# Kernel tuning notes

Measured on AMD Instinct MI355X. Metric: run time of the kernel, lower is better.

## Reference

```python
import jax, jax.numpy as jnp
import numpy as np

N = 50000        # nodes
E = 800000       # edges
G = 256          # graphs in batch
DIMS = [128, 128, 64, 32]
BN_EPS = 1e-5
TEMP = 5.0


def setup_inputs() -> dict:
    key = jax.random.key(0)
    ks = iter(jax.random.split(key, 32))
    inp = {}
    inp["x"] = jax.random.normal(next(ks), (N, DIMS[0]), dtype=jnp.float32)
    inp["edge_index"] = jax.random.randint(next(ks), (2, E), 0, N)
    inp["batch"] = jnp.sort(jax.random.randint(next(ks), (N,), 0, G))
    for i in range(3):
        din, dout = DIMS[i], DIMS[i + 1]
        inp[f"W1_{i}"] = jax.random.normal(next(ks), (din, dout), dtype=jnp.float32) * 0.05
        inp[f"b1_{i}"] = jnp.zeros((dout,), jnp.float32)
        inp[f"W2_{i}"] = jax.random.normal(next(ks), (dout, dout), dtype=jnp.float32) * 0.05
        inp[f"b2_{i}"] = jnp.zeros((dout,), jnp.float32)
        inp[f"gamma_{i}"] = jnp.ones((dout,), jnp.float32)
        inp[f"beta_{i}"] = jnp.zeros((dout,), jnp.float32)
        inp[f"mean_{i}"] = jnp.zeros((dout,), jnp.float32)
        inp[f"var_{i}"] = jnp.ones((dout,), jnp.float32)
    inp["W_lin"] = jax.random.normal(next(ks), (DIMS[3], 1), dtype=jnp.float32) * 0.05
    inp["b_lin"] = jnp.zeros((1,), jnp.float32)
    return inp


def _gin_bn(x, src, dst, W1, b1, W2, b2, g, b, m, v):
    # GINConv with eps=0: h_i = MLP(x_i + sum_{j->i} x_j), then BatchNorm (eval)
    agg = jax.ops.segment_sum(x[src], dst, num_segments=N)  # [N, din]
    h = x + agg
    h = jnp.maximum(h @ W1 + b1, 0.0) @ W2 + b2             # 2-layer MLP
    return (h - m) * jax.lax.rsqrt(v + BN_EPS) * g + b


def reference(x, edge_index, batch,
              W1_0, b1_0, W2_0, b2_0, gamma_0, beta_0, mean_0, var_0,
              W1_1, b1_1, W2_1, b2_1, gamma_1, beta_1, mean_1, var_1,
              W1_2, b1_2, W2_2, b2_2, gamma_2, beta_2, mean_2, var_2,
              W_lin, b_lin):
    src, dst = edge_index[0], edge_index[1]
    layers = [
        (W1_0, b1_0, W2_0, b2_0, gamma_0, beta_0, mean_0, var_0),
        (W1_1, b1_1, W2_1, b2_1, gamma_1, beta_1, mean_1, var_1),
        (W1_2, b1_2, W2_2, b2_2, gamma_2, beta_2, mean_2, var_2),
    ]
    for i, p in enumerate(layers):
        x = _gin_bn(x, src, dst, *p)
        if i != len(layers) - 1:
            x = jnp.maximum(x, 0.0)  # relu; dropout is identity in eval mode
    logits = (x @ W_lin + b_lin) / TEMP                      # [N, 1]
    # per-graph (segment) softmax over nodes
    mx = jax.ops.segment_max(logits, batch, num_segments=G)  # [G, 1]
    e = jnp.exp(logits - mx[batch])
    s = jax.ops.segment_sum(e, batch, num_segments=G)        # [G, 1]
    return e / s[batch]
```

## Files before the change

### kernel.cpp

```cpp
#include <hip/hip_runtime.h>

#define NN 50000
#define NE 800000
#define NG 256
#define NB ((NN + 255) / 256)
#define N4 (NN * 128 / 4)

typedef __attribute__((ext_vector_type(8))) short bf16x8;
typedef __attribute__((ext_vector_type(4))) float f32x4;

__device__ __forceinline__ unsigned short f2bf_rne(float f) {
    unsigned u = __float_as_uint(f);
    u += 0x7fffu + ((u >> 16) & 1u);
    return (unsigned short)(u >> 16);
}
#define BF2F_LO(u) __uint_as_float((u) << 16)
#define BF2F_HI(u) __uint_as_float((u) & 0xffff0000u)

__global__ void conv_hist(const float4* __restrict__ x, ushort4* __restrict__ xh,
                          const int* __restrict__ dst, int* __restrict__ deg,
                          int* __restrict__ eoff) {
    int i = blockIdx.x * 256 + threadIdx.x;
    if (i < N4) {
        float4 v = x[i];
        ushort4 o;
        o.x = f2bf_rne(v.x); o.y = f2bf_rne(v.y);
        o.z = f2bf_rne(v.z); o.w = f2bf_rne(v.w);
        xh[i] = o;
    }
    if (i < NE) eoff[i] = atomicAdd(&deg[dst[i]], 1);
}

__global__ void block_scan(const int* __restrict__ deg, int* __restrict__ iscan,
                           int* __restrict__ bsum,
                           const float* __restrict__ W1, const float* __restrict__ W2,
                           const float* __restrict__ W3,
                           const float* __restrict__ W21, const float* __restrict__ W12,
                           unsigned short* __restrict__ W1t,
                           unsigned short* __restrict__ W2t,
                           unsigned short* __restrict__ W3t,
                           unsigned short* __restrict__ W21t,
                           unsigned short* __restrict__ W12t) {
    int gidx = blockIdx.x * 256 + threadIdx.x;
    if (gidx < 16384) {
        int n = gidx >> 7, k = gidx & 127;
        W1t[gidx] = f2bf_rne(W1[k * 128 + n]);
        W2t[gidx] = f2bf_rne(W2[k * 128 + n]);
    } else if (gidx < 24576) {
        int i2 = gidx - 16384;
        int n = i2 >> 7, k = i2 & 127;
        W3t[i2] = f2bf_rne(W3[k * 64 + n]);
    } else if (gidx < 28672) {
        int i3 = gidx - 24576;
        int n = i3 >> 6, k = i3 & 63;
        W21t[i3] = f2bf_rne(W21[k * 64 + n]);
    } else if (gidx < 30720) {
        int i4 = gidx - 28672;
        int n = i4 >> 6, k = i4 & 63;
        W12t[i4] = f2bf_rne(W12[k * 32 + n]);
    }

    __shared__ int sh[256];
    int t = threadIdx.x;
    int i = blockIdx.x * 256 + t;
    int v = (i < NN) ? deg[i] : 0;
    sh[t] = v;
    __syncthreads();
    #pragma unroll
    for (int off = 1; off < 256; off <<= 1) {
        int add = (t >= off) ? sh[t - off] : 0;
        __syncthreads();
        sh[t] += add;
        __syncthreads();
    }
    if (i < NN) iscan[i] = sh[t];
    if (t == 255) bsum[blockIdx.x] = sh[255];
}

__global__ void scan_bsum(const int* __restrict__ bsum, int* __restrict__ boff) {
    __shared__ int sh[256];
    int t = threadIdx.x;
    int v = (t < NB) ? bsum[t] : 0;
    sh[t] = v;
    __syncthreads();
    #pragma unroll
    for (int off = 1; off < 256; off <<= 1) {
        int add = (t >= off) ? sh[t - off] : 0;
        __syncthreads();
        sh[t] += add;
        __syncthreads();
    }
    if (t < NB) boff[t] = sh[t] - v;
}

__global__ void finalize_bounds(const int* __restrict__ deg, const int* __restrict__ iscan,
                                const int* __restrict__ boff, int* __restrict__ rowptr,
                                const int* __restrict__ batch, int* __restrict__ gstart) {
    int i = blockIdx.x * 256 + threadIdx.x;
    if (i < NN) {
        rowptr[i] = iscan[i] - deg[i] + boff[blockIdx.x];
        int b = batch[i];
        if (i == 0) {
            for (int g = 0; g <= b; g++) gstart[g] = 0;
        } else {
            int p = batch[i - 1];
            for (int g = p + 1; g <= b; g++) gstart[g] = i;
        }
        if (i == NN - 1) {
            for (int g = b + 1; g <= NG; g++) gstart[g] = NN;
        }
    }
    if (i == 0) rowptr[NN] = NE;
}

__global__ void fill_csr2(const int* __restrict__ src, const int* __restrict__ dst,
                          const int* __restrict__ rowptr, const int* __restrict__ eoff,
                          int* __restrict__ esrc) {
    int e = blockIdx.x * blockDim.x + threadIdx.x;
    if (e >= NE) return;
    esrc[rowptr[dst[e]] + eoff[e]] = src[e];
}


template <int C4>
__device__ __forceinline__ void gather_bf16(const uint4* __restrict__ x4,
                                            const int* __restrict__ esrc,
                                            int beg, int cnt, int node, int lane,
                                            float* a ) {
    constexpr int EPI = 64 / C4;
    const int chunk = lane & (C4 - 1);
    const int esl   = lane / C4;
    #define ACC_U4(u) do { \
        a[0] += BF2F_LO((u).x); a[1] += BF2F_HI((u).x); \
        a[2] += BF2F_LO((u).y); a[3] += BF2F_HI((u).y); \
        a[4] += BF2F_LO((u).z); a[5] += BF2F_HI((u).z); \
        a[6] += BF2F_LO((u).w); a[7] += BF2F_HI((u).w); } while (0)
    if (esl == 0) { uint4 u = x4[(size_t)node * C4 + chunk]; ACC_U4(u); }
    for (int c = 0; c < cnt; c += 64) {
        int take = min(64, cnt - c);
        int myi = (lane < take) ? esrc[beg + c + lane] : 0;
        int i = 0;
        for (; i + 4 * EPI <= take; i += 4 * EPI) {
            int s0 = __shfl(myi, i + esl);
            int s1 = __shfl(myi, i + EPI + esl);
            int s2 = __shfl(myi, i + 2 * EPI + esl);
            int s3 = __shfl(myi, i + 3 * EPI + esl);
            uint4 u0 = x4[(size_t)s0 * C4 + chunk];
            uint4 u1 = x4[(size_t)s1 * C4 + chunk];
            uint4 u2 = x4[(size_t)s2 * C4 + chunk];
            uint4 u3 = x4[(size_t)s3 * C4 + chunk];
            ACC_U4(u0); ACC_U4(u1); ACC_U4(u2); ACC_U4(u3);
        }
        if (i + 2 * EPI <= take) {
            int s0 = __shfl(myi, i + esl);
            int s1 = __shfl(myi, i + EPI + esl);
            uint4 u0 = x4[(size_t)s0 * C4 + chunk];
            uint4 u1 = x4[(size_t)s1 * C4 + chunk];
            ACC_U4(u0); ACC_U4(u1);
            i += 2 * EPI;
        }
        if (i + EPI <= take) {
            int s = __shfl(myi, i + esl);
            uint4 u = x4[(size_t)s * C4 + chunk];
            ACC_U4(u);
            i += EPI;
        }
        int rem = take - i;
        if (rem > 0) {
            int s = __shfl(myi, i + ((esl < rem) ? esl : 0));
            uint4 u = x4[(size_t)s * C4 + chunk];
            if (esl < rem) ACC_U4(u);
        }
    }
    #undef ACC_U4
    for (int off = 32; off >= C4; off >>= 1) {
        #pragma unroll
        for (int q = 0; q < 8; q++)
            a[q] += __shfl_xor(a[q], off);
    }
}

template <int C>
__device__ __forceinline__ void gather_bf16_u2(const uint2* __restrict__ x2,
                                               const int* __restrict__ esrc,
                                               int beg, int cnt, int node, int lane,
                                               float* a ) {
    constexpr int EPI = 64 / C;
    const int chunk = lane & (C - 1);
    const int esl   = lane / C;
    #define ACC_U2(u) do { \
        a[0] += BF2F_LO((u).x); a[1] += BF2F_HI((u).x); \
        a[2] += BF2F_LO((u).y); a[3] += BF2F_HI((u).y); } while (0)
    if (esl == 0) { uint2 u = x2[(size_t)node * C + chunk]; ACC_U2(u); }
    for (int c = 0; c < cnt; c += 64) {
        int take = min(64, cnt - c);
        int myi = (lane < take) ? esrc[beg + c + lane] : 0;
        int i = 0;
        for (; i + 4 * EPI <= take; i += 4 * EPI) {
            int s0 = __shfl(myi, i + esl);
            int s1 = __shfl(myi, i + EPI + esl);
            int s2 = __shfl(myi, i + 2 * EPI + esl);
            int s3 = __shfl(myi, i + 3 * EPI + esl);
            uint2 u0 = x2[(size_t)s0 * C + chunk];
            uint2 u1 = x2[(size_t)s1 * C + chunk];
            uint2 u2 = x2[(size_t)s2 * C + chunk];
            uint2 u3 = x2[(size_t)s3 * C + chunk];
            ACC_U2(u0); ACC_U2(u1); ACC_U2(u2); ACC_U2(u3);
        }
        if (i + 2 * EPI <= take) {
            int s0 = __shfl(myi, i + esl);
            int s1 = __shfl(myi, i + EPI + esl);
            uint2 u0 = x2[(size_t)s0 * C + chunk];
            uint2 u1 = x2[(size_t)s1 * C + chunk];
            ACC_U2(u0); ACC_U2(u1);
            i += 2 * EPI;
        }
        if (i + EPI <= take) {
            int s = __shfl(myi, i + esl);
            uint2 u = x2[(size_t)s * C + chunk];
            ACC_U2(u);
            i += EPI;
        }
        int rem = take - i;
        if (rem > 0) {
            int s = __shfl(myi, i + ((esl < rem) ? esl : 0));
            uint2 u = x2[(size_t)s * C + chunk];
            if (esl < rem) ACC_U2(u);
        }
    }
    #undef ACC_U2
    for (int off = 32; off >= C; off >>= 1) {
        #pragma unroll
        for (int q = 0; q < 4; q++)
            a[q] += __shfl_xor(a[q], off);
    }
}

template <int C>
__device__ __forceinline__ void gather_bf16_u1(const unsigned* __restrict__ x1,
                                               const int* __restrict__ esrc,
                                               int beg, int cnt, int node, int lane,
                                               float* a ) {
    constexpr int EPI = 64 / C;
    const int chunk = lane & (C - 1);
    const int esl   = lane / C;
    #define ACC_U1(u) do { \
        a[0] += BF2F_LO(u); a[1] += BF2F_HI(u); } while (0)
    if (esl == 0) { unsigned u = x1[(size_t)node * C + chunk]; ACC_U1(u); }
    for (int c = 0; c < cnt; c += 64) {
        int take = min(64, cnt - c);
        int myi = (lane < take) ? esrc[beg + c + lane] : 0;
        int i = 0;
        for (; i + 4 * EPI <= take; i += 4 * EPI) {
            int s0 = __shfl(myi, i + esl);
            int s1 = __shfl(myi, i + EPI + esl);
            int s2 = __shfl(myi, i + 2 * EPI + esl);
            int s3 = __shfl(myi, i + 3 * EPI + esl);
            unsigned u0 = x1[(size_t)s0 * C + chunk];
            unsigned u1 = x1[(size_t)s1 * C + chunk];
            unsigned u2 = x1[(size_t)s2 * C + chunk];
            unsigned u3 = x1[(size_t)s3 * C + chunk];
            ACC_U1(u0); ACC_U1(u1); ACC_U1(u2); ACC_U1(u3);
        }
        if (i + 2 * EPI <= take) {
            int s0 = __shfl(myi, i + esl);
            int s1 = __shfl(myi, i + EPI + esl);
            unsigned u0 = x1[(size_t)s0 * C + chunk];
            unsigned u1 = x1[(size_t)s1 * C + chunk];
            ACC_U1(u0); ACC_U1(u1);
            i += 2 * EPI;
        }
        if (i + EPI <= take) {
            int s = __shfl(myi, i + esl);
            unsigned u = x1[(size_t)s * C + chunk];
            ACC_U1(u);
            i += EPI;
        }
        int rem = take - i;
        if (rem > 0) {
            int s = __shfl(myi, i + ((esl < rem) ? esl : 0));
            unsigned u = x1[(size_t)s * C + chunk];
            if (esl < rem) ACC_U1(u);
        }
    }
    #undef ACC_U1
    for (int off = 32; off >= C; off >>= 1) {
        #pragma unroll
        for (int q = 0; q < 2; q++)
            a[q] += __shfl_xor(a[q], off);
    }
}

__global__ __launch_bounds__(256) void gather_L0(
        const unsigned short* __restrict__ xh, const int* __restrict__ esrc,
        const int* __restrict__ rowptr, unsigned short* __restrict__ aggh ) {
    const int wave = threadIdx.x >> 6, lane = threadIdx.x & 63;
    const int node = blockIdx.x * 4 + wave;
    if (node >= NN) return;
    float a[8] = {0, 0, 0, 0, 0, 0, 0, 0};
    int beg = rowptr[node], end = rowptr[node + 1];
    gather_bf16<16>((const uint4*)xh, esrc, beg, end - beg, node, lane, a);
    if (lane < 16) {
        uint4 o;
        o.x = (unsigned)f2bf_rne(a[0]) | ((unsigned)f2bf_rne(a[1]) << 16);
        o.y = (unsigned)f2bf_rne(a[2]) | ((unsigned)f2bf_rne(a[3]) << 16);
        o.z = (unsigned)f2bf_rne(a[4]) | ((unsigned)f2bf_rne(a[5]) << 16);
        o.w = (unsigned)f2bf_rne(a[6]) | ((unsigned)f2bf_rne(a[7]) << 16);
        *(uint4*)&aggh[(size_t)node * 128 + lane * 8] = o;
    }
}

__global__ __launch_bounds__(256) void gather_L1(
        const unsigned short* __restrict__ z1h, const int* __restrict__ esrc,
        const int* __restrict__ rowptr, const float* __restrict__ b1,
        unsigned short* __restrict__ agg1h ) {
    const int wave = threadIdx.x >> 6, lane = threadIdx.x & 63;
    const int node = blockIdx.x * 4 + wave;
    if (node >= NN) return;
    float a[4] = {0, 0, 0, 0};
    int beg = rowptr[node], end = rowptr[node + 1];
    gather_bf16_u2<16>((const uint2*)z1h, esrc, beg, end - beg, node, lane, a);
    if (lane < 16) {
        float4 bv = *(const float4*)&b1[lane * 4];
        uint2 o;
        o.x = (unsigned)f2bf_rne(fmaxf(a[0] + bv.x, 0.f)) |
              ((unsigned)f2bf_rne(fmaxf(a[1] + bv.y, 0.f)) << 16);
        o.y = (unsigned)f2bf_rne(fmaxf(a[2] + bv.z, 0.f)) |
              ((unsigned)f2bf_rne(fmaxf(a[3] + bv.w, 0.f)) << 16);
        *(uint2*)&agg1h[(size_t)node * 64 + lane * 4] = o;
    }
}

__global__ __launch_bounds__(256) void gather_L2(
        const unsigned short* __restrict__ z2h, const int* __restrict__ esrc,
        const int* __restrict__ rowptr, const float* __restrict__ b1,
        unsigned short* __restrict__ agg2h ) {
    const int wave = threadIdx.x >> 6, lane = threadIdx.x & 63;
    const int node = blockIdx.x * 4 + wave;
    if (node >= NN) return;
    float a[2] = {0, 0};
    int beg = rowptr[node], end = rowptr[node + 1];
    gather_bf16_u1<16>((const unsigned*)z2h, esrc, beg, end - beg, node, lane, a);
    if (lane < 16) {
        float2 bv = *(const float2*)&b1[lane * 2];
        unsigned o = (unsigned)f2bf_rne(fmaxf(a[0] + bv.x, 0.f)) |
                     ((unsigned)f2bf_rne(fmaxf(a[1] + bv.y, 0.f)) << 16);
        *(unsigned*)&agg2h[(size_t)node * 32 + lane * 2] = o;
    }
}

__global__ __launch_bounds__(256) void gemm_L0(
        const unsigned short* __restrict__ aggh, unsigned short* __restrict__ z1h,
        const unsigned short* __restrict__ W1t,
        const unsigned short* __restrict__ W2t,
        const unsigned short* __restrict__ W3t,
        const float* __restrict__ b1, const float* __restrict__ b2,
        const float* __restrict__ gamma, const float* __restrict__ beta,
        const float* __restrict__ mean, const float* __restrict__ var) {
    constexpr int MT = 64, LDA = 136;
    __shared__ __align__(16) unsigned short shA[MT * LDA];
    __shared__ __align__(16) unsigned short shB[MT * LDA];
    const int tid = threadIdx.x;
    const int wave = tid >> 6, lane = tid & 63;
    const int nodeBase = blockIdx.x * MT;
    const int lr = lane & 15;
    const int lg = lane >> 4;
    const int lk = lg * 8;
    const int n0 = wave * 32;

    #pragma unroll
    for (int j = 0; j < 4; j++) {
        int f = tid + j * 256;
        int row = f >> 4, c = f & 15;
        int node = nodeBase + row;
        uint4 v = (node < NN) ? ((const uint4*)aggh)[(size_t)node * 16 + c]
                              : make_uint4(0u, 0u, 0u, 0u);
        *(uint4*)&shA[row * LDA + c * 8] = v;
    }
    __syncthreads();

    f32x4 acc[4][2];

    {
        float bv0 = b1[n0 + lr], bv1 = b1[n0 + 16 + lr];
        #pragma unroll
        for (int m = 0; m < 4; m++) {
            f32x4 c0 = {bv0, bv0, bv0, bv0};
            f32x4 c1 = {bv1, bv1, bv1, bv1};
            acc[m][0] = c0; acc[m][1] = c1;
        }
        #pragma unroll
        for (int ks = 0; ks < 4; ks++) {
            const int k0 = ks * 32 + lk;
            bf16x8 wb0 = *(const bf16x8*)&W1t[(n0 + lr) * 128 + k0];
            bf16x8 wb1 = *(const bf16x8*)&W1t[(n0 + 16 + lr) * 128 + k0];
            #pragma unroll
            for (int m = 0; m < 4; m++) {
                bf16x8 af = *(const bf16x8*)&shA[(m * 16 + lr) * LDA + k0];
                acc[m][0] = __builtin_amdgcn_mfma_f32_16x16x32_bf16(af, wb0, acc[m][0], 0, 0, 0);
                acc[m][1] = __builtin_amdgcn_mfma_f32_16x16x32_bf16(af, wb1, acc[m][1], 0, 0, 0);
            }
        }
    }
    #pragma unroll
    for (int m = 0; m < 4; m++) {
        #pragma unroll
        for (int nt = 0; nt < 2; nt++) {
            #pragma unroll
            for (int r = 0; r < 4; r++) {
                shB[(m * 16 + lg * 4 + r) * LDA + (n0 + nt * 16 + lr)] =
                    f2bf_rne(fmaxf(acc[m][nt][r], 0.f));
            }
        }
    }
    __syncthreads();

    {
        float bv0 = b2[n0 + lr], bv1 = b2[n0 + 16 + lr];
        #pragma unroll
        for (int m = 0; m < 4; m++) {
            f32x4 c0 = {bv0, bv0, bv0, bv0};
            f32x4 c1 = {bv1, bv1, bv1, bv1};
            acc[m][0] = c0; acc[m][1] = c1;
        }
        #pragma unroll
        for (int ks = 0; ks < 4; ks++) {
            const int k0 = ks * 32 + lk;
            bf16x8 wb0 = *(const bf16x8*)&W2t[(n0 + lr) * 128 + k0];
            bf16x8 wb1 = *(const bf16x8*)&W2t[(n0 + 16 + lr) * 128 + k0];
            #pragma unroll
            for (int m = 0; m < 4; m++) {
                bf16x8 af = *(const bf16x8*)&shB[(m * 16 + lr) * LDA + k0];
                acc[m][0] = __builtin_amdgcn_mfma_f32_16x16x32_bf16(af, wb0, acc[m][0], 0, 0, 0);
                acc[m][1] = __builtin_amdgcn_mfma_f32_16x16x32_bf16(af, wb1, acc[m][1], 0, 0, 0);
            }
        }
    }
    float s0 = gamma[n0 + lr]      * (1.0f / sqrtf(var[n0 + lr] + 1e-5f));
    float t0 = beta[n0 + lr]       - mean[n0 + lr] * s0;
    float s1 = gamma[n0 + 16 + lr] * (1.0f / sqrtf(var[n0 + 16 + lr] + 1e-5f));
    float t1 = beta[n0 + 16 + lr]  - mean[n0 + 16 + lr] * s1;
    #pragma unroll
    for (int m = 0; m < 4; m++) {
        #pragma unroll
        for (int nt = 0; nt < 2; nt++) {
            float sc = nt ? s1 : s0, sf = nt ? t1 : t0;
            #pragma unroll
            for (int r = 0; r < 4; r++) {
                float y = fmaxf(fmaf(acc[m][nt][r], sc, sf), 0.f);
                shA[(m * 16 + lg * 4 + r) * LDA + (n0 + nt * 16 + lr)] = f2bf_rne(y);
            }
        }
    }
    __syncthreads();

    f32x4 a3[4];
    #pragma unroll
    for (int m = 0; m < 4; m++) {
        f32x4 z = {0.f, 0.f, 0.f, 0.f};
        a3[m] = z;
    }
    #pragma unroll
    for (int ks = 0; ks < 4; ks++) {
        const int k0 = ks * 32 + lk;
        bf16x8 wb = *(const bf16x8*)&W3t[(wave * 16 + lr) * 128 + k0];
        #pragma unroll
        for (int m = 0; m < 4; m++) {
            bf16x8 af = *(const bf16x8*)&shA[(m * 16 + lr) * LDA + k0];
            a3[m] = __builtin_amdgcn_mfma_f32_16x16x32_bf16(af, wb, a3[m], 0, 0, 0);
        }
    }
    #pragma unroll
    for (int m = 0; m < 4; m++) {
        #pragma unroll
        for (int r = 0; r < 4; r++) {
            int node = nodeBase + m * 16 + lg * 4 + r;
            if (node < NN)
                z1h[(size_t)node * 64 + wave * 16 + lr] = f2bf_rne(a3[m][r]);
        }
    }
}

__global__ __launch_bounds__(256) void gemm_L1(
        const unsigned short* __restrict__ agg1h, unsigned short* __restrict__ z2h,
        const unsigned short* __restrict__ W21t,
        const unsigned short* __restrict__ W12t,
        const float* __restrict__ b2, const float* __restrict__ gamma,
        const float* __restrict__ beta, const float* __restrict__ mean,
        const float* __restrict__ var) {
    constexpr int MT = 64, LDA = 72;
    __shared__ __align__(16) unsigned short shA[MT * LDA];
    __shared__ __align__(16) unsigned short shB[MT * LDA];
    const int tid = threadIdx.x;
    const int wave = tid >> 6, lane = tid & 63;
    const int nodeBase = blockIdx.x * MT;
    const int lr = lane & 15;
    const int lg = lane >> 4;
    const int lk = lg * 8;
    const int n0 = wave * 16;

    #pragma unroll
    for (int j = 0; j < 2; j++) {
        int f = tid + j * 256;
        int row = f >> 3, c = f & 7;
        int node = nodeBase + row;
        uint4 v = (node < NN) ? ((const uint4*)agg1h)[(size_t)node * 8 + c]
                              : make_uint4(0u, 0u, 0u, 0u);
        *(uint4*)&shA[row * LDA + c * 8] = v;
    }
    __syncthreads();

    f32x4 acc[4];
    {
        float bv = b2[n0 + lr];
        #pragma unroll
        for (int m = 0; m < 4; m++) {
            f32x4 c0 = {bv, bv, bv, bv};
            acc[m] = c0;
        }
        #pragma unroll
        for (int ks = 0; ks < 2; ks++) {
            const int k0 = ks * 32 + lk;
            bf16x8 wb = *(const bf16x8*)&W21t[(n0 + lr) * 64 + k0];
            #pragma unroll
            for (int m = 0; m < 4; m++) {
                bf16x8 af = *(const bf16x8*)&shA[(m * 16 + lr) * LDA + k0];
                acc[m] = __builtin_amdgcn_mfma_f32_16x16x32_bf16(af, wb, acc[m], 0, 0, 0);
            }
        }
    }
    float sc = gamma[n0 + lr] * (1.0f / sqrtf(var[n0 + lr] + 1e-5f));
    float sf = beta[n0 + lr] - mean[n0 + lr] * sc;
    #pragma unroll
    for (int m = 0; m < 4; m++) {
        #pragma unroll
        for (int r = 0; r < 4; r++) {
            float y = fmaxf(fmaf(acc[m][r], sc, sf), 0.f);
            shB[(m * 16 + lg * 4 + r) * LDA + (n0 + lr)] = f2bf_rne(y);
        }
    }
    __syncthreads();

    const int rh = (wave >> 1) * 32, ch = (wave & 1) * 16;
    f32x4 a3[2];
    {
        f32x4 z = {0.f, 0.f, 0.f, 0.f};
        a3[0] = z; a3[1] = z;
    }
    #pragma unroll
    for (int ks = 0; ks < 2; ks++) {
        const int k0 = ks * 32 + lk;
        bf16x8 wb = *(const bf16x8*)&W12t[(ch + lr) * 64 + k0];
        #pragma unroll
        for (int m = 0; m < 2; m++) {
            bf16x8 af = *(const bf16x8*)&shB[(rh + m * 16 + lr) * LDA + k0];
            a3[m] = __builtin_amdgcn_mfma_f32_16x16x32_bf16(af, wb, a3[m], 0, 0, 0);
        }
    }
    #pragma unroll
    for (int m = 0; m < 2; m++) {
        #pragma unroll
        for (int r = 0; r < 4; r++) {
            int node = nodeBase + rh + m * 16 + lg * 4 + r;
            if (node < NN)
                z2h[(size_t)node * 32 + ch + lr] = f2bf_rne(a3[m][r]);
        }
    }
}

__global__ __launch_bounds__(256) void gemm_L2(
        const unsigned short* __restrict__ agg2h, float* __restrict__ logits,
        const float* __restrict__ W2, const float* __restrict__ b2,
        const float* __restrict__ gamma, const float* __restrict__ beta,
        const float* __restrict__ mean, const float* __restrict__ var,
        const float* __restrict__ Wl, const float* __restrict__ bl) {
    constexpr int MT = 32, LD = 36;
    __shared__ float sh[MT * LD];
    const int tid = threadIdx.x;
    const int nodeBase = blockIdx.x * MT;

    {
        int row = tid >> 3, c = tid & 7;
        int node = nodeBase + row;
        uint2 v = (node < NN) ? ((const uint2*)agg2h)[(size_t)node * 8 + c]
                              : make_uint2(0u, 0u);
        sh[row * LD + c * 4 + 0] = BF2F_LO(v.x);
        sh[row * LD + c * 4 + 1] = BF2F_HI(v.x);
        sh[row * LD + c * 4 + 2] = BF2F_LO(v.y);
        sh[row * LD + c * 4 + 3] = BF2F_HI(v.y);
    }
    __syncthreads();

    const int colid = tid % 8, rowid = tid / 8;
    const int c0 = colid * 4, r0 = rowid;
    float acc[4];
    {
        float4 bv = *(const float4*)&b2[c0];
        acc[0] = bv.x; acc[1] = bv.y; acc[2] = bv.z; acc[3] = bv.w;
        #pragma unroll
        for (int k4 = 0; k4 < 8; k4++) {
            float4 w[4];
            #pragma unroll
            for (int kk = 0; kk < 4; kk++)
                w[kk] = *(const float4*)&W2[(k4 * 4 + kk) * 32 + c0];
            float4 a = *(const float4*)&sh[r0 * LD + k4 * 4];
            const float av[4] = {a.x, a.y, a.z, a.w};
            #pragma unroll
            for (int kk = 0; kk < 4; kk++) {
                const float* wp = (const float*)&w[kk];
                #pragma unroll
                for (int j = 0; j < 4; j++)
                    acc[j] = fmaf(av[kk], wp[j], acc[j]);
            }
        }
    }
    float4 gv = *(const float4*)&gamma[c0];
    float4 bev = *(const float4*)&beta[c0];
    float4 mv = *(const float4*)&mean[c0];
    float4 vv = *(const float4*)&var[c0];
    float4 wl = *(const float4*)&Wl[c0];
    float p = 0.f;
    {
        const float* gp = (const float*)&gv; const float* bp = (const float*)&bev;
        const float* mp = (const float*)&mv; const float* vp = (const float*)&vv;
        const float* wp = (const float*)&wl;
        #pragma unroll
        for (int j = 0; j < 4; j++) {
            float sc = gp[j] * (1.0f / sqrtf(vp[j] + 1e-5f));
            float y = (acc[j] - mp[j]) * sc + bp[j];
            p = fmaf(y, wp[j], p);
        }
    }
    p += __shfl_xor(p, 1);
    p += __shfl_xor(p, 2);
    p += __shfl_xor(p, 4);
    int node = nodeBase + r0;
    if ((tid & 7) == 0 && node < NN)
        logits[node] = (p + bl[0]) * 0.2f;
}

__global__ __launch_bounds__(256) void seg_softmax(
        const float* __restrict__ logits, const int* __restrict__ gstart,
        float* __restrict__ out) {
    __shared__ float slog[1024];
    __shared__ float sred[4];
    __shared__ float sbc[2];
    int g = blockIdx.x;
    int beg = gstart[g], end = gstart[g + 1];
    int cnt = end - beg;
    int t = threadIdx.x;
    if (cnt <= 0) return;
    bool fits = (cnt <= 1024);

    float lmax = -3.402823466e+38f;
    for (int i = t; i < cnt; i += 256) {
        float lg = logits[beg + i];
        if (fits) slog[i] = lg;
        lmax = fmaxf(lmax, lg);
    }
    #pragma unroll
    for (int off = 32; off > 0; off >>= 1)
        lmax = fmaxf(lmax, __shfl_down(lmax, off));
    if ((t & 63) == 0) sred[t >> 6] = lmax;
    __syncthreads();
    if (t == 0) sbc[0] = fmaxf(fmaxf(sred[0], sred[1]), fmaxf(sred[2], sred[3]));
    __syncthreads();
    float gm = sbc[0];

    float lsum = 0.f;
    for (int i = t; i < cnt; i += 256) {
        float lg = fits ? slog[i] : logits[beg + i];
        float e = expf(lg - gm);
        if (fits) slog[i] = e;
        lsum += e;
    }
    #pragma unroll
    for (int off = 32; off > 0; off >>= 1)
        lsum += __shfl_down(lsum, off);
    __syncthreads();
    if ((t & 63) == 0) sred[t >> 6] = lsum;
    __syncthreads();
    if (t == 0) sbc[1] = (sred[0] + sred[1]) + (sred[2] + sred[3]);
    __syncthreads();
    float inv = 1.0f / sbc[1];

    for (int i = t; i < cnt; i += 256) {
        float e = fits ? slog[i] : expf(logits[beg + i] - gm);
        out[beg + i] = e * inv;
    }
}

extern "C" void kernel_launch(void* const* d_in, const int* in_sizes, int n_in,
                              void* d_out, int out_size, void* d_ws, size_t ws_size,
                              hipStream_t stream) {
    const float* x    = (const float*)d_in[0];
    const int*   ei   = (const int*)d_in[1];
    const int*   srcI = ei;
    const int*   dstI = ei + NE;
    const int*   batch = (const int*)d_in[2];

    const float* P[29];
    for (int i = 0; i < 29; i++) P[i] = (const float*)d_in[i];
    const float* Wlin = P[27];
    const float* blin = P[28];

    unsigned short* xh  = (unsigned short*)d_ws;
    unsigned short* z1h = xh + (size_t)NN * 128;
    unsigned short* z2h = z1h + (size_t)NN * 64;
    float* logits = (float*)(z2h + (size_t)NN * 32);
    int* gstart = (int*)(logits + NN);
    int* deg    = gstart + NG + 1;
    int* iscan  = deg + NN;
    int* rowptr = iscan + NN;
    int* bsum   = rowptr + NN + 1;
    int* boff   = bsum + NB;
    int* eoff   = boff + NB;
    int* esrc   = eoff + NE;
    uintptr_t pal = ((uintptr_t)(esrc + NE) + 255) & ~(uintptr_t)255;
    unsigned short* aggh  = (unsigned short*)pal;
    unsigned short* W1t   = aggh + (size_t)NN * 128;
    unsigned short* W2t   = W1t + 16384;
    unsigned short* W3t   = W2t + 16384;
    unsigned short* W21t  = W3t + 8192;
    unsigned short* W12t  = W21t + 4096;
    unsigned short* agg1h = W12t + 2048;
    unsigned short* agg2h = agg1h + (size_t)NN * 64;
    float* outp = (float*)d_out;

    const int TB = 256;

    hipMemsetAsync(deg, 0, NN * sizeof(int), stream);
    conv_hist<<<(N4 + TB - 1) / TB, TB, 0, stream>>>(
        (const float4*)x, (ushort4*)xh, dstI, deg, eoff);

    block_scan<<<NB, 256, 0, stream>>>(deg, iscan, bsum,
        P[3], P[5], P[11], P[13], P[19], W1t, W2t, W3t, W21t, W12t);
    scan_bsum<<<1, 256, 0, stream>>>(bsum, boff);
    finalize_bounds<<<NB, 256, 0, stream>>>(deg, iscan, boff, rowptr, batch, gstart);
    fill_csr2<<<(NE + TB - 1) / TB, TB, 0, stream>>>(srcI, dstI, rowptr, eoff, esrc);

    const int GB   = (NN + 3) / 4;
    const int FB64 = (NN + 63) / 64;
    const int FB32 = (NN + 31) / 32;

    gather_L0<<<GB, 256, 0, stream>>>(xh, esrc, rowptr, aggh);
    gemm_L0<<<FB64, 256, 0, stream>>>(aggh, z1h, W1t, W2t, W3t,
        P[4], P[6], P[7], P[8], P[9], P[10]);
    gather_L1<<<GB, 256, 0, stream>>>(z1h, esrc, rowptr, P[12], agg1h);
    gemm_L1<<<FB64, 256, 0, stream>>>(agg1h, z2h, W21t, W12t,
        P[14], P[15], P[16], P[17], P[18]);
    gather_L2<<<GB, 256, 0, stream>>>(z2h, esrc, rowptr, P[20], agg2h);
    gemm_L2<<<FB32, 256, 0, stream>>>(agg2h, logits,
        P[21], P[22], P[23], P[24], P[25], P[26], Wlin, blin);

    seg_softmax<<<NG, 256, 0, stream>>>(logits, gstart, outp);
}
```

Measured before the change: 285.6 us.

## Build CSR with two-pass bucketed counting sort using shared-memory atomics

Replaces the global-atomic degree histogram, three-kernel scan and random scatter with a two-level radix-style counting sort. Edges are first bucketed by dst>>8 into 196 coarse buckets using per-block shared-memory histograms, then each bucket block sorts its edges by the low 8 bits locally and writes rowptr and esrc. This removes global atomic contention and the memset, at the cost of an extra (src,dst) temp buffer pass and a serial single-block scan. Edge order within a row becomes nondeterministic but the sum is order-insensitive up to float rounding.

Measured after the change: 262.3 us. 1.09x faster.

```diff
diff --git a/kernel.cpp b/kernel.cpp
--- a/kernel.cpp
+++ b/kernel.cpp
@@ -3,8 +3,11 @@
 #define NN 50000
 #define NE 800000
 #define NG 256
-#define NB ((NN + 255) / 256)
 #define N4 (NN * 128 / 4)
+#define NQ (NE / 4)
+#define CB 64
+#define QPB (NQ / CB)
+#define NBK 196
 
 typedef __attribute__((ext_vector_type(8))) short bf16x8;
 typedef __attribute__((ext_vector_type(4))) float f32x4;
@@ -17,9 +20,9 @@
 #define BF2F_LO(u) __uint_as_float((u) << 16)
 #define BF2F_HI(u) __uint_as_float((u) & 0xffff0000u)
 
-__global__ void conv_hist(const float4* __restrict__ x, ushort4* __restrict__ xh,
-                          const int* __restrict__ dst, int* __restrict__ deg,
-                          int* __restrict__ eoff) {
+__global__ void conv_count(const float4* __restrict__ x, ushort4* __restrict__ xh,
+                           const int4* __restrict__ dst4, int* __restrict__ cnt1) {
+    __shared__ int hist[NBK];
     int i = blockIdx.x * 256 + threadIdx.x;
     if (i < N4) {
         float4 v = x[i];
@@ -28,19 +31,91 @@
         o.z = f2bf_rne(v.z); o.w = f2bf_rne(v.w);
         xh[i] = o;
     }
-    if (i < NE) eoff[i] = atomicAdd(&deg[dst[i]], 1);
-}
-
-__global__ void block_scan(const int* __restrict__ deg, int* __restrict__ iscan,
-                           int* __restrict__ bsum,
-                           const float* __restrict__ W1, const float* __restrict__ W2,
-                           const float* __restrict__ W3,
-                           const float* __restrict__ W21, const float* __restrict__ W12,
-                           unsigned short* __restrict__ W1t,
-                           unsigned short* __restrict__ W2t,
-                           unsigned short* __restrict__ W3t,
-                           unsigned short* __restrict__ W21t,
-                           unsigned short* __restrict__ W12t) {
+    if (blockIdx.x < CB) {
+        int t = threadIdx.x;
+        if (t < NBK) hist[t] = 0;
+        __syncthreads();
+        int qb = blockIdx.x * QPB;
+        for (int qi = t; qi < QPB; qi += 256) {
+            int4 d = dst4[qb + qi];
+            atomicAdd(&hist[d.x >> 8], 1);
+            atomicAdd(&hist[d.y >> 8], 1);
+            atomicAdd(&hist[d.z >> 8], 1);
+            atomicAdd(&hist[d.w >> 8], 1);
+        }
+        __syncthreads();
+        if (t < NBK) cnt1[blockIdx.x * NBK + t] = hist[t];
+    }
+}
+
+__global__ __launch_bounds__(256) void scan_buckets(
+        const int* __restrict__ cnt1, int* __restrict__ off1,
+        int* __restrict__ bstart, int* __restrict__ rowptr) {
+    __shared__ int c[CB * NBK];
+    __shared__ int sh[256];
+    int t = threadIdx.x;
+    for (int idx = t; idx < CB * NBK; idx += 256) c[idx] = cnt1[idx];
+    __syncthreads();
+    int tot = 0;
+    if (t < NBK) {
+        for (int b = 0; b < CB; b++) {
+            int v = c[b * NBK + t];
+            c[b * NBK + t] = tot;
+            tot += v;
+        }
+    }
+    sh[t] = (t < NBK) ? tot : 0;
+    __syncthreads();
+    int v = sh[t];
+    #pragma unroll
+    for (int off = 1; off < 256; off <<= 1) {
+        int add = (t >= off) ? sh[t - off] : 0;
+        __syncthreads();
+        sh[t] += add;
+        __syncthreads();
+    }
+    int excl = sh[t] - v;
+    if (t < NBK) {
+        bstart[t] = excl;
+        for (int b = 0; b < CB; b++) c[b * NBK + t] += excl;
+    }
+    if (t == 0) { bstart[NBK] = NE; rowptr[NN] = NE; }
+    __syncthreads();
+    for (int idx = t; idx < CB * NBK; idx += 256) off1[idx] = c[idx];
+}
+
+__global__ __launch_bounds__(256) void scatter1(
+        const int4* __restrict__ src4, const int4* __restrict__ dst4,
+        const int* __restrict__ off1, int2* __restrict__ tmp) {
+    __shared__ int curs[NBK];
+    int t = threadIdx.x;
+    if (t < NBK) curs[t] = off1[blockIdx.x * NBK + t];
+    __syncthreads();
+    int qb = blockIdx.x * QPB;
+    for (int qi = t; qi < QPB; qi += 256) {
+        int4 s = src4[qb + qi];
+        int4 d = dst4[qb + qi];
+        int p0 = atomicAdd(&curs[d.x >> 8], 1);
+        int p1 = atomicAdd(&curs[d.y >> 8], 1);
+        int p2 = atomicAdd(&curs[d.z >> 8], 1);
+        int p3 = atomicAdd(&curs[d.w >> 8], 1);
+        tmp[p0] = make_int2(s.x, d.x);
+        tmp[p1] = make_int2(s.y, d.y);
+        tmp[p2] = make_int2(s.z, d.z);
+        tmp[p3] = make_int2(s.w, d.w);
+    }
+}
+
+__global__ __launch_bounds__(256) void bucket_build(
+        const int2* __restrict__ tmp, const int* __restrict__ bstart,
+        const int* __restrict__ batch, int* __restrict__ rowptr,
+        int* __restrict__ gstart, int* __restrict__ esrc,
+        const float* __restrict__ W1, const float* __restrict__ W2,
+        const float* __restrict__ W3,
+        const float* __restrict__ W21, const float* __restrict__ W12,
+        unsigned short* __restrict__ W1t, unsigned short* __restrict__ W2t,
+        unsigned short* __restrict__ W3t, unsigned short* __restrict__ W21t,
+        unsigned short* __restrict__ W12t) {
     int gidx = blockIdx.x * 256 + threadIdx.x;
     if (gidx < 16384) {
         int n = gidx >> 7, k = gidx & 127;
@@ -60,10 +135,20 @@
         W12t[i4] = f2bf_rne(W12[k * 32 + n]);
     }
 
+    __shared__ int hist[256];
     __shared__ int sh[256];
-    int t = threadIdx.x;
-    int i = blockIdx.x * 256 + t;
-    int v = (i < NN) ? deg[i] : 0;
+    __shared__ int curs[256];
+    int t = threadIdx.x, k1 = blockIdx.x;
+    int b0 = bstart[k1], b1v = bstart[k1 + 1];
+    int cnt = b1v - b0;
+    hist[t] = 0;
+    __syncthreads();
+    for (int e = t; e < cnt; e += 256) {
+        int2 sd = tmp[b0 + e];
+        atomicAdd(&hist[sd.y & 255], 1);
+    }
+    __syncthreads();
+    int v = hist[t];
     sh[t] = v;
     __syncthreads();
     #pragma unroll
@@ -73,52 +158,28 @@
         sh[t] += add;
         __syncthreads();
     }
-    if (i < NN) iscan[i] = sh[t];
-    if (t == 255) bsum[blockIdx.x] = sh[255];
-}
-
-__global__ void scan_bsum(const int* __restrict__ bsum, int* __restrict__ boff) {
-    __shared__ int sh[256];
-    int t = threadIdx.x;
-    int v = (t < NB) ? bsum[t] : 0;
-    sh[t] = v;
-    __syncthreads();
-    #pragma unroll
-    for (int off = 1; off < 256; off <<= 1) {
-        int add = (t >= off) ? sh[t - off] : 0;
-        __syncthreads();
-        sh[t] += add;
-        __syncthreads();
-    }
-    if (t < NB) boff[t] = sh[t] - v;
-}
-
-__global__ void finalize_bounds(const int* __restrict__ deg, const int* __restrict__ iscan,
-                                const int* __restrict__ boff, int* __restrict__ rowptr,
-                                const int* __restrict__ batch, int* __restrict__ gstart) {
-    int i = blockIdx.x * 256 + threadIdx.x;
-    if (i < NN) {
-        rowptr[i] = iscan[i] - deg[i] + boff[blockIdx.x];
-        int b = batch[i];
-        if (i == 0) {
+    int excl = sh[t] - v;
+    int node = k1 * 256 + t;
+    if (node < NN) {
+        rowptr[node] = b0 + excl;
+        int b = batch[node];
+        if (node == 0) {
             for (int g = 0; g <= b; g++) gstart[g] = 0;
         } else {
-            int p = batch[i - 1];
-            for (int g = p + 1; g <= b; g++) gstart[g] = i;
-        }
-        if (i == NN - 1) {
+            int p = batch[node - 1];
+            for (int g = p + 1; g <= b; g++) gstart[g] = node;
+        }
+        if (node == NN - 1) {
             for (int g = b + 1; g <= NG; g++) gstart[g] = NN;
         }
     }
-    if (i == 0) rowptr[NN] = NE;
-}
-
-__global__ void fill_csr2(const int* __restrict__ src, const int* __restrict__ dst,
-                          const int* __restrict__ rowptr, const int* __restrict__ eoff,
-                          int* __restrict__ esrc) {
-    int e = blockIdx.x * blockDim.x + threadIdx.x;
-    if (e >= NE) return;
-    esrc[rowptr[dst[e]] + eoff[e]] = src[e];
+    curs[t] = b0 + excl;
+    __syncthreads();
+    for (int e = t; e < cnt; e += 256) {
+        int2 sd = tmp[b0 + e];
+        int slot = atomicAdd(&curs[sd.y & 255], 1);
+        esrc[slot] = sd.x;
+    }
 }
 
 
@@ -709,13 +770,13 @@
     unsigned short* z2h = z1h + (size_t)NN * 64;
     float* logits = (float*)(z2h + (size_t)NN * 32);
     int* gstart = (int*)(logits + NN);
-    int* deg    = gstart + NG + 1;
-    int* iscan  = deg + NN;
-    int* rowptr = iscan + NN;
-    int* bsum   = rowptr + NN + 1;
-    int* boff   = bsum + NB;
-    int* eoff   = boff + NB;
-    int* esrc   = eoff + NE;
+    int* rowptr = gstart + NG + 1;
+    int* cnt1   = rowptr + NN + 1;
+    int* off1   = cnt1 + CB * NBK;
+    int* bstart = off1 + CB * NBK;
+    uintptr_t tal = ((uintptr_t)(bstart + NBK + 1) + 15) & ~(uintptr_t)15;
+    int2* tmp   = (int2*)tal;
+    int* esrc   = (int*)(tmp + NE);
     uintptr_t pal = ((uintptr_t)(esrc + NE) + 255) & ~(uintptr_t)255;
     unsigned short* aggh  = (unsigned short*)pal;
     unsigned short* W1t   = aggh + (size_t)NN * 128;
@@ -729,15 +790,13 @@
 
     const int TB = 256;
 
-    hipMemsetAsync(deg, 0, NN * sizeof(int), stream);
-    conv_hist<<<(N4 + TB - 1) / TB, TB, 0, stream>>>(
-        (const float4*)x, (ushort4*)xh, dstI, deg, eoff);
-
-    block_scan<<<NB, 256, 0, stream>>>(deg, iscan, bsum,
+    conv_count<<<(N4 + TB - 1) / TB, TB, 0, stream>>>(
+        (const float4*)x, (ushort4*)xh, (const int4*)dstI, cnt1);
+    scan_buckets<<<1, 256, 0, stream>>>(cnt1, off1, bstart, rowptr);
+    scatter1<<<CB, 256, 0, stream>>>(
+        (const int4*)srcI, (const int4*)dstI, off1, tmp);
+    bucket_build<<<NBK, 256, 0, stream>>>(tmp, bstart, batch, rowptr, gstart, esrc,
         P[3], P[5], P[11], P[13], P[19], W1t, W2t, W3t, W21t, W12t);
-    scan_bsum<<<1, 256, 0, stream>>>(bsum, boff);
-    finalize_bounds<<<NB, 256, 0, stream>>>(deg, iscan, boff, rowptr, batch, gstart);
-    fill_csr2<<<(NE + TB - 1) / TB, TB, 0, stream>>>(srcI, dstI, rowptr, eoff, esrc);
 
     const int GB   = (NN + 3) / 4;
     const int FB64 = (NN + 63) / 64;
```
